# Performance work log

Measured on AMD Instinct MI355X. Metric: run time of the kernel, lower is better.

Reference implementation:

```python
import jax, jax.numpy as jnp
import numpy as np


def setup_inputs() -> dict:
    key = jax.random.key(0)
    k1, k2, k3, k4 = jax.random.split(key, 4)
    B, S, d_in, d_out = 4, 2048, 1024, 1024
    scale = 1.0 / np.sqrt(d_in)
    x = jax.random.normal(k1, (B, S, d_in), dtype=jnp.float32)
    # Linear weights stored as [d_in, d_out] so projection is x @ W
    Wq = jax.random.normal(k2, (d_in, d_out), dtype=jnp.float32) * scale
    Wk = jax.random.normal(k3, (d_in, d_out), dtype=jnp.float32) * scale
    Wv = jax.random.normal(k4, (d_in, d_out), dtype=jnp.float32) * scale
    return {"x": x, "Wq": Wq, "Wk": Wk, "Wv": Wv}


def reference(x, Wq, Wk, Wv):
    # QKV projections (no bias, matching qkv_bias=False)
    q = jnp.einsum("bsi,io->bso", x, Wq)
    k = jnp.einsum("bsi,io->bso", x, Wk)
    v = jnp.einsum("bsi,io->bso", x, Wv)
    d_k = k.shape[-1]
    # attn_scores = q @ k^T, causal mask (strict upper triangle -> -inf)
    scores = jnp.einsum("bqd,bkd->bqk", q, k)
    S = scores.shape[-1]
    causal = jnp.tril(jnp.ones((S, S), dtype=bool))  # True where allowed
    scores = jnp.where(causal, scores, -jnp.inf)
    attn = jax.nn.softmax(scores / jnp.sqrt(jnp.asarray(d_k, scores.dtype)), axis=-1)
    # dropout p=0.0 -> identity
    return jnp.einsum("bqk,bkd->bqd", attn, v)
```

## Files before the change

kernel.cpp:

```cpp
#include <hip/hip_runtime.h>

typedef _Float16 half8 __attribute__((ext_vector_type(8)));
typedef _Float16 half4 __attribute__((ext_vector_type(4)));
typedef float f32x4 __attribute__((ext_vector_type(4)));

#define ATT_SCALE 0.03125f
#define S_LEN 2048
#define D_DIM 1024
#define NB 4

__device__ __forceinline__ void async_cp16(const _Float16* g, _Float16* l)
{
    __builtin_amdgcn_global_load_lds(
        (const __attribute__((address_space(1))) void*)g,
        (__attribute__((address_space(3))) void*)l, 16, 0, 0);
}

__device__ __forceinline__ void gemm_core(const _Float16* __restrict__ Ag,
                                          const _Float16* __restrict__ Bg,
                                          int lda, int ldb, int ksteps,
                                          f32x4 acc[4][4])
{
    __shared__ _Float16 As[128 * 32];
    __shared__ _Float16 Bs[128 * 32];

    const int t    = threadIdx.x;
    const int wave = t >> 6;
    const int lane = t & 63;
    const int wm   = (wave >> 1) * 64;
    const int wn   = (wave & 1) * 64;
    const int lg   = lane >> 4;
    const int lr   = lane & 15;

    const int c0 = t,        r0 = c0 >> 2, h0 = (c0 & 3) * 8;
    const int c1 = 256 + t,  r1 = c1 >> 2, h1 = (c1 & 3) * 8;
    const int lb0 = (wave * 64) * 8;
    const int lb1 = (256 + wave * 64) * 8;

    const _Float16* a0p = Ag + (long)r0 * lda + h0;
    const _Float16* a1p = Ag + (long)r1 * lda + h1;
    const _Float16* b0p = Bg + (long)r0 * ldb + h0;
    const _Float16* b1p = Bg + (long)r1 * ldb + h1;

    for (int ks = 0; ks < ksteps; ++ks) {
        __syncthreads();
        async_cp16(a0p, As + lb0);
        async_cp16(a1p, As + lb1);
        async_cp16(b0p, Bs + lb0);
        async_cp16(b1p, Bs + lb1);
        __syncthreads();

        a0p += 32; a1p += 32; b0p += 32; b1p += 32;

        half8 af[4], bf[4];
#pragma unroll
        for (int i = 0; i < 4; ++i)
            af[i] = *(const half8*)&As[(wm + i * 16 + lr) * 32 + lg * 8];
#pragma unroll
        for (int j = 0; j < 4; ++j)
            bf[j] = *(const half8*)&Bs[(wn + j * 16 + lr) * 32 + lg * 8];

#pragma unroll
        for (int i = 0; i < 4; ++i)
#pragma unroll
            for (int j = 0; j < 4; ++j)
                acc[i][j] = __builtin_amdgcn_mfma_f32_16x16x32_f16(af[i], bf[j], acc[i][j], 0, 0, 0);
    }
}

__global__ void zero_sums_kernel(float* __restrict__ rs)
{
    rs[blockIdx.x * 256 + threadIdx.x] = 0.f;
}

__global__ void zero_out_kernel(float4* __restrict__ p, long n4)
{
    const float4 z = {0.f, 0.f, 0.f, 0.f};
    for (long i = (long)blockIdx.x * blockDim.x + threadIdx.x; i < n4;
         i += (long)gridDim.x * blockDim.x)
        p[i] = z;
}

__global__ void cast_x_kernel(const float* __restrict__ X, _Float16* __restrict__ Xh, int n)
{
    int i = blockIdx.x * blockDim.x + threadIdx.x;
    if (i * 4 >= n) return;
    float4 v = ((const float4*)X)[i];
    half4 h;
    h.x = (_Float16)v.x; h.y = (_Float16)v.y; h.z = (_Float16)v.z; h.w = (_Float16)v.w;
    ((half4*)Xh)[i] = h;
}

__global__ void transpose_w_kernel(const float* __restrict__ Wq,
                                   const float* __restrict__ Wk,
                                   const float* __restrict__ Wv,
                                   _Float16* __restrict__ Wt)
{
    __shared__ float tile[32][33];
    const int n0 = blockIdx.x * 32, k0 = blockIdx.y * 32, w = blockIdx.z;
    const float* Wsrc = (w == 0) ? Wq : (w == 1) ? Wk : Wv;
    _Float16* dst = Wt + (long)w * D_DIM * D_DIM;
    const int tx = threadIdx.x, ty = threadIdx.y;
#pragma unroll
    for (int j = 0; j < 4; ++j)
        tile[ty + 8 * j][tx] = Wsrc[(long)(k0 + ty + 8 * j) * D_DIM + n0 + tx];
    __syncthreads();
#pragma unroll
    for (int j = 0; j < 4; ++j)
        dst[(long)(n0 + ty + 8 * j) * D_DIM + k0 + tx] = (_Float16)tile[tx][ty + 8 * j];
}

__global__ __launch_bounds__(256) void proj_kernel(const _Float16* __restrict__ Xh,
                                                   const _Float16* __restrict__ Wt,
                                                   _Float16* __restrict__ Q,
                                                   _Float16* __restrict__ K,
                                                   _Float16* __restrict__ V)
{
    const int flat = blockIdx.x + 8 * (blockIdx.y + 64 * blockIdx.z);
    const int swz  = (flat & 7) * 192 + (flat >> 3);
    const int nt = swz & 7, mt = (swz >> 3) & 63, w = swz >> 9;

    f32x4 acc[4][4];
#pragma unroll
    for (int i = 0; i < 4; ++i)
#pragma unroll
        for (int j = 0; j < 4; ++j) acc[i][j] = (f32x4){0.f, 0.f, 0.f, 0.f};

    const _Float16* Ag = Xh + (long)mt * 128 * D_DIM;
    const _Float16* Bg = Wt + (long)w * D_DIM * D_DIM + (long)nt * 128 * D_DIM;
    gemm_core(Ag, Bg, D_DIM, D_DIM, D_DIM / 32, acc);

    _Float16* C = (w == 0) ? Q : (w == 1) ? K : V;
    const int t = threadIdx.x, wave = t >> 6, lane = t & 63;
    const int wm = (wave >> 1) * 64, wn = (wave & 1) * 64;
    const int lg = lane >> 4, lr = lane & 15;
    const long row0 = (long)mt * 128 + wm + 4 * lg;
    const long col0 = (long)nt * 128 + wn + lr;
#pragma unroll
    for (int i = 0; i < 4; ++i)
#pragma unroll
        for (int j = 0; j < 4; ++j)
#pragma unroll
            for (int r = 0; r < 4; ++r)
                C[(row0 + i * 16 + r) * D_DIM + col0 + j * 16] = (_Float16)acc[i][j][r];
}

__global__ __launch_bounds__(256) void transpose_v_kernel(const _Float16* __restrict__ V,
                                                          _Float16* __restrict__ Vt)
{
    __shared__ _Float16 tile[64][72];
    const int d0 = blockIdx.x * 64, s0 = blockIdx.y * 64;
    const long b = blockIdx.z;
    const _Float16* Vb = V + b * S_LEN * D_DIM;
    _Float16* Vtb = Vt + b * D_DIM * S_LEN;
    const int t = threadIdx.x;
    const int sr = t >> 3, c8 = (t & 7) * 8;

    *(half8*)&tile[sr][c8]      = *(const half8*)&Vb[(long)(s0 + sr) * D_DIM + d0 + c8];
    *(half8*)&tile[sr + 32][c8] = *(const half8*)&Vb[(long)(s0 + sr + 32) * D_DIM + d0 + c8];
    __syncthreads();

    const int dr = t >> 3, s8 = (t & 7) * 8;
    half8 o0, o1;
#pragma unroll
    for (int e = 0; e < 8; ++e) {
        o0[e] = tile[s8 + e][dr];
        o1[e] = tile[s8 + e][dr + 32];
    }
    *(half8*)&Vtb[(long)(d0 + dr) * S_LEN + s0 + s8]      = o0;
    *(half8*)&Vtb[(long)(d0 + dr + 32) * S_LEN + s0 + s8] = o1;
}

__global__ __launch_bounds__(256) void scores_exp_kernel(const _Float16* __restrict__ Q,
                                                         const _Float16* __restrict__ K,
                                                         _Float16* __restrict__ P,
                                                         float* __restrict__ row_sum)
{
    const int xcd = blockIdx.x & 7;
    const int idx = blockIdx.x >> 3;
    const int b   = idx / 17;
    const int l   = idx % 17;
    int qt, kt;
    if (l <= xcd) { qt = xcd;      kt = l; }
    else          { qt = 15 - xcd; kt = l - xcd - 1; }

    f32x4 acc[4][4];
#pragma unroll
    for (int i = 0; i < 4; ++i)
#pragma unroll
        for (int j = 0; j < 4; ++j) acc[i][j] = (f32x4){0.f, 0.f, 0.f, 0.f};

    const _Float16* Ag = Q + ((long)b * S_LEN + qt * 128) * D_DIM;
    const _Float16* Bg = K + ((long)b * S_LEN + kt * 128) * D_DIM;
    gemm_core(Ag, Bg, D_DIM, D_DIM, D_DIM / 32, acc);

    _Float16* Pb = P + (long)b * S_LEN * S_LEN;
    float* rsb = row_sum + (long)b * S_LEN;
    const int t = threadIdx.x, wave = t >> 6, lane = t & 63;
    const int wm = (wave >> 1) * 64, wn = (wave & 1) * 64;
    const int lg = lane >> 4, lr = lane & 15;
    const int row0 = qt * 128 + wm + 4 * lg;
    const int col0 = kt * 128 + wn + lr;

#pragma unroll
    for (int i = 0; i < 4; ++i) {
#pragma unroll
        for (int r = 0; r < 4; ++r) {
            const int row = row0 + i * 16 + r;
            float s = 0.f;
#pragma unroll
            for (int j = 0; j < 4; ++j) {
                const int col = col0 + j * 16;
                float p = (col <= row) ? __expf(acc[i][j][r] * ATT_SCALE) : 0.f;
                s += p;
                Pb[(long)row * S_LEN + col] = (_Float16)p;
            }
#pragma unroll
            for (int off = 1; off < 16; off <<= 1) s += __shfl_xor(s, off, 64);
            if (lr == 0) atomicAdd(&rsb[row], s);
        }
    }
}

__global__ __launch_bounds__(256) void pv_kernel(const _Float16* __restrict__ P,
                                                 const _Float16* __restrict__ Vt,
                                                 const float* __restrict__ row_sum,
                                                 float* __restrict__ O)
{
    const int xcd = blockIdx.x & 7;
    int r = blockIdx.x >> 3;
    const int b = r / 24;  r %= 24;
    const int j = r >> 3;
    const int nt = r & 7;
    const int sl = (j == 0) ? (7 - xcd) : (j == 1 ? 8 + 2 * xcd : 9 + 2 * xcd);

    int qt, k0s, ks;
    if (sl < 8) { qt = sl; k0s = 0; ks = (qt + 1) * 4; }
    else {
        const int e = sl - 8;
        qt = 8 + (e >> 1);
        ks = (qt + 1) * 2;
        k0s = (e & 1) * ks;
    }

    f32x4 acc[4][4];
#pragma unroll
    for (int i = 0; i < 4; ++i)
#pragma unroll
        for (int jj = 0; jj < 4; ++jj) acc[i][jj] = (f32x4){0.f, 0.f, 0.f, 0.f};

    const _Float16* Ag = P + ((long)b * S_LEN + qt * 128) * S_LEN + k0s * 32;
    const _Float16* Bg = Vt + (long)b * D_DIM * S_LEN + (long)nt * 128 * S_LEN + k0s * 32;
    gemm_core(Ag, Bg, S_LEN, S_LEN, ks, acc);

    float* Ob = O + (long)b * S_LEN * D_DIM;
    const float* rsb = row_sum + (long)b * S_LEN;
    const int t = threadIdx.x, wave = t >> 6, lane = t & 63;
    const int wm = (wave >> 1) * 64, wn = (wave & 1) * 64;
    const int lg = lane >> 4, lr = lane & 15;
    const long row0 = qt * 128 + wm + 4 * lg;
    const long col0 = (long)nt * 128 + wn + lr;

    if (sl < 8) {
#pragma unroll
        for (int i = 0; i < 4; ++i)
#pragma unroll
            for (int rr = 0; rr < 4; ++rr) {
                const float inv = 1.f / rsb[row0 + i * 16 + rr];
#pragma unroll
                for (int jj = 0; jj < 4; ++jj)
                    Ob[(row0 + i * 16 + rr) * D_DIM + col0 + jj * 16] = acc[i][jj][rr] * inv;
            }
    } else {
#pragma unroll
        for (int i = 0; i < 4; ++i)
#pragma unroll
            for (int rr = 0; rr < 4; ++rr) {
                const float inv = 1.f / rsb[row0 + i * 16 + rr];
#pragma unroll
                for (int jj = 0; jj < 4; ++jj)
                    atomicAdd(&Ob[(row0 + i * 16 + rr) * D_DIM + col0 + jj * 16],
                              acc[i][jj][rr] * inv);
            }
    }
}

extern "C" void kernel_launch(void* const* d_in, const int* in_sizes, int n_in,
                              void* d_out, int out_size, void* d_ws, size_t ws_size,
                              hipStream_t stream)
{
    const float* x  = (const float*)d_in[0];
    const float* Wq = (const float*)d_in[1];
    const float* Wk = (const float*)d_in[2];
    const float* Wv = (const float*)d_in[3];
    float* out = (float*)d_out;

    char* ws = (char*)d_ws;
    const long MiB = 1024 * 1024;
    _Float16* Q  = (_Float16*)(ws + 0 * MiB);
    _Float16* K  = (_Float16*)(ws + 16 * MiB);
    _Float16* V  = (_Float16*)(ws + 32 * MiB);
    _Float16* Vt = (_Float16*)(ws + 48 * MiB);
    _Float16* Xh = (_Float16*)(ws + 64 * MiB);
    _Float16* Wt = (_Float16*)(ws + 80 * MiB);
    _Float16* P  = (_Float16*)(ws + 86 * MiB);
    float*    RS = (float*)   (ws + 118 * MiB);

    const int nX = in_sizes[0];

    zero_sums_kernel<<<dim3(NB * S_LEN / 256), dim3(256), 0, stream>>>(RS);
    zero_out_kernel<<<dim3(2048), dim3(256), 0, stream>>>((float4*)out,
                                                          (long)NB * S_LEN * D_DIM / 4);
    cast_x_kernel<<<dim3((nX / 4 + 255) / 256), dim3(256), 0, stream>>>(x, Xh, nX);
    transpose_w_kernel<<<dim3(32, 32, 3), dim3(32, 8), 0, stream>>>(Wq, Wk, Wv, Wt);
    proj_kernel<<<dim3(8, 64, 3), dim3(256), 0, stream>>>(Xh, Wt, Q, K, V);
    transpose_v_kernel<<<dim3(16, 32, 4), dim3(256), 0, stream>>>(V, Vt);
    scores_exp_kernel<<<dim3(544), dim3(256), 0, stream>>>(Q, K, P, RS);
    pv_kernel<<<dim3(768), dim3(256), 0, stream>>>(P, Vt, RS, out);
}
```

Measured before the change: 187.6 us.

## Rewrite QKV projection GEMM with 256x256 tiles and double-buffered swizzled LDS

The projection kernel moves from a 128x128 tile with 256 threads to a 256x256 tile with 512 threads (8 waves). It stages 64-wide K slices through double-buffered LDS with async global-to-LDS copies and an XOR swizzle, raises wave priority around the MFMA bursts, and remaps blocks to improve L2 reuse. The goal is more arithmetic per byte loaded and load latency hidden behind MFMA work. In exchange it uses 128 KB of LDS and many more accumulator registers per block, and it launches only 384 blocks, which may leave some CUs without work.

```diff
diff --git a/kernel.cpp b/kernel.cpp
--- a/kernel.cpp
+++ b/kernel.cpp
@@ -110,39 +110,111 @@
         dst[(long)(n0 + ty + 8 * j) * D_DIM + k0 + tx] = (_Float16)tile[tx][ty + 8 * j];
 }
 
-__global__ __launch_bounds__(256) void proj_kernel(const _Float16* __restrict__ Xh,
-                                                   const _Float16* __restrict__ Wt,
-                                                   _Float16* __restrict__ Q,
-                                                   _Float16* __restrict__ K,
-                                                   _Float16* __restrict__ V)
-{
-    const int flat = blockIdx.x + 8 * (blockIdx.y + 64 * blockIdx.z);
-    const int swz  = (flat & 7) * 192 + (flat >> 3);
-    const int nt = swz & 7, mt = (swz >> 3) & 63, w = swz >> 9;
-
-    f32x4 acc[4][4];
-#pragma unroll
-    for (int i = 0; i < 4; ++i)
+__global__ __launch_bounds__(512, 2) void proj_kernel(const _Float16* __restrict__ Xh,
+                                                      const _Float16* __restrict__ Wt,
+                                                      _Float16* __restrict__ Q,
+                                                      _Float16* __restrict__ K,
+                                                      _Float16* __restrict__ V)
+{
+    __shared__ _Float16 As[2][256 * 64];
+    __shared__ _Float16 Bs[2][256 * 64];
+
+    const int bid = blockIdx.x;
+    const int g   = (bid & 7) * 48 + (bid >> 3);
+    const int mt  = g / 12;
+    const int rem = g % 12;
+    const int w   = rem >> 2;
+    const int nt  = rem & 3;
+
+    const int t    = threadIdx.x;
+    const int wave = t >> 6;
+    const int lane = t & 63;
+    const int wr   = wave >> 2;
+    const int wc   = wave & 3;
+    const int lg   = lane >> 4;
+    const int lr   = lane & 15;
+
+    const _Float16* Ag = Xh + (long)mt * 256 * D_DIM;
+    const _Float16* Bg = Wt + (long)w * D_DIM * D_DIM + (long)nt * 256 * D_DIM;
+
+    const int rsel = lane >> 3;
+    const int csel = ((lane & 7) ^ rsel) * 8;
+    const int w8   = wave * 8;
+    const int ldst = wave * 512;
+
+#define STAGE_TILE(dstA, dstB, kt1)                                             \
+    {                                                                           \
+        _Pragma("unroll")                                                       \
+        for (int i_ = 0; i_ < 4; ++i_)                                          \
+            async_cp16(Ag + (long)(i_ * 64 + w8 + rsel) * D_DIM + (kt1) * 64 + csel, \
+                       (dstA) + i_ * 4096 + ldst);                              \
+        _Pragma("unroll")                                                       \
+        for (int i_ = 0; i_ < 4; ++i_)                                          \
+            async_cp16(Bg + (long)(i_ * 64 + w8 + rsel) * D_DIM + (kt1) * 64 + csel, \
+                       (dstB) + i_ * 4096 + ldst);                              \
+    }
+
+    f32x4 acc[8][4];
+#pragma unroll
+    for (int i = 0; i < 8; ++i)
 #pragma unroll
         for (int j = 0; j < 4; ++j) acc[i][j] = (f32x4){0.f, 0.f, 0.f, 0.f};
 
-    const _Float16* Ag = Xh + (long)mt * 128 * D_DIM;
-    const _Float16* Bg = Wt + (long)w * D_DIM * D_DIM + (long)nt * 128 * D_DIM;
-    gemm_core(Ag, Bg, D_DIM, D_DIM, D_DIM / 32, acc);
+    STAGE_TILE(As[0], Bs[0], 0);
+
+    const int cswz = (lr & 7) << 4;
+    const int nkt  = D_DIM / 64;
+
+    for (int kt = 0; kt < nkt; ++kt) {
+        const int d = kt & 1;
+        if (kt > 0) __builtin_amdgcn_s_barrier();
+        if (kt + 1 < nkt) {
+            STAGE_TILE(As[d ^ 1], Bs[d ^ 1], kt + 1);
+            asm volatile("s_waitcnt vmcnt(8)" ::: "memory");
+        } else {
+            asm volatile("s_waitcnt vmcnt(0)" ::: "memory");
+        }
+        __builtin_amdgcn_s_barrier();
+
+        const char* Ab = (const char*)As[d];
+        const char* Bb = (const char*)Bs[d];
+#pragma unroll
+        for (int kh = 0; kh < 2; ++kh) {
+            const int cb = (kh * 64 + lg * 16) ^ cswz;
+            half8 bf[4];
+#pragma unroll
+            for (int j = 0; j < 4; ++j)
+                bf[j] = *(const half8*)(Bb + (wc * 64 + j * 16 + lr) * 128 + cb);
+#pragma unroll
+            for (int mh = 0; mh < 2; ++mh) {
+                half8 af[4];
+#pragma unroll
+                for (int i = 0; i < 4; ++i)
+                    af[i] = *(const half8*)(Ab + (wr * 128 + (mh * 4 + i) * 16 + lr) * 128 + cb);
+                __builtin_amdgcn_s_setprio(1);
+#pragma unroll
+                for (int i = 0; i < 4; ++i)
+#pragma unroll
+                    for (int j = 0; j < 4; ++j)
+                        acc[mh * 4 + i][j] = __builtin_amdgcn_mfma_f32_16x16x32_f16(
+                            af[i], bf[j], acc[mh * 4 + i][j], 0, 0, 0);
+                __builtin_amdgcn_s_setprio(0);
+                if (!(kh == 1 && mh == 1)) __builtin_amdgcn_s_barrier();
+            }
+        }
+    }
+#undef STAGE_TILE
 
     _Float16* C = (w == 0) ? Q : (w == 1) ? K : V;
-    const int t = threadIdx.x, wave = t >> 6, lane = t & 63;
-    const int wm = (wave >> 1) * 64, wn = (wave & 1) * 64;
-    const int lg = lane >> 4, lr = lane & 15;
-    const long row0 = (long)mt * 128 + wm + 4 * lg;
-    const long col0 = (long)nt * 128 + wn + lr;
-#pragma unroll
-    for (int i = 0; i < 4; ++i)
+    const long row0 = (long)mt * 256 + wr * 128 + lg * 4;
+    const long col0 = (long)nt * 256 + wc * 64 + lr;
+#pragma unroll
+    for (int mf = 0; mf < 8; ++mf)
 #pragma unroll
         for (int j = 0; j < 4; ++j)
 #pragma unroll
-            for (int r = 0; r < 4; ++r)
-                C[(row0 + i * 16 + r) * D_DIM + col0 + j * 16] = (_Float16)acc[i][j][r];
+            for (int rr = 0; rr < 4; ++rr)
+                C[(row0 + mf * 16 + rr) * D_DIM + col0 + j * 16] = (_Float16)acc[mf][j][rr];
 }
 
 __global__ __launch_bounds__(256) void transpose_v_kernel(const _Float16* __restrict__ V,
@@ -313,7 +385,7 @@
                                                           (long)NB * S_LEN * D_DIM / 4);
     cast_x_kernel<<<dim3((nX / 4 + 255) / 256), dim3(256), 0, stream>>>(x, Xh, nX);
     transpose_w_kernel<<<dim3(32, 32, 3), dim3(32, 8), 0, stream>>>(Wq, Wk, Wv, Wt);
-    proj_kernel<<<dim3(8, 64, 3), dim3(256), 0, stream>>>(Xh, Wt, Q, K, V);
+    proj_kernel<<<dim3(384), dim3(512), 0, stream>>>(Xh, Wt, Q, K, V);
     transpose_v_kernel<<<dim3(16, 32, 4), dim3(256), 0, stream>>>(V, Vt);
     scores_exp_kernel<<<dim3(544), dim3(256), 0, stream>>>(Q, K, P, RS);
     pv_kernel<<<dim3(768), dim3(256), 0, stream>>>(P, Vt, RS, out);
```

New measurement: 199.4 us. +6.3%, slower.

## Double GEMM K-tile to 64 with XOR-swizzled LDS and fuse init kernels

Applied to the files above, without the earlier changes.

The shared GEMM core now loads 64-wide K slices per iteration instead of 32. This halves the number of barrier pairs per tile and doubles the MFMA work between syncs. LDS rows are XOR-swizzled to avoid bank conflicts on the wider rows. The three init kernels (zero row sums, zero output, cast x) are merged into one launch, and the projection grid is flattened to 1D. The cost is twice the LDS use per block, which may lower occupancy.

```diff
diff --git a/kernel.cpp b/kernel.cpp
--- a/kernel.cpp
+++ b/kernel.cpp
@@ -16,13 +16,13 @@
         (__attribute__((address_space(3))) void*)l, 16, 0, 0);
 }
 
-__device__ __forceinline__ void gemm_core(const _Float16* __restrict__ Ag,
-                                          const _Float16* __restrict__ Bg,
-                                          int lda, int ldb, int ksteps,
-                                          f32x4 acc[4][4])
-{
-    __shared__ _Float16 As[128 * 32];
-    __shared__ _Float16 Bs[128 * 32];
+__device__ __forceinline__ void gemm_core64(const _Float16* __restrict__ Ag,
+                                            const _Float16* __restrict__ Bg,
+                                            int lda, int ldb, int ksteps64,
+                                            f32x4 acc[4][4])
+{
+    __shared__ _Float16 As[128 * 64];
+    __shared__ _Float16 Bs[128 * 64];
 
     const int t    = threadIdx.x;
     const int wave = t >> 6;
@@ -32,63 +32,72 @@
     const int lg   = lane >> 4;
     const int lr   = lane & 15;
 
-    const int c0 = t,        r0 = c0 >> 2, h0 = (c0 & 3) * 8;
-    const int c1 = 256 + t,  r1 = c1 >> 2, h1 = (c1 & 3) * 8;
-    const int lb0 = (wave * 64) * 8;
-    const int lb1 = (256 + wave * 64) * 8;
-
-    const _Float16* a0p = Ag + (long)r0 * lda + h0;
-    const _Float16* a1p = Ag + (long)r1 * lda + h1;
-    const _Float16* b0p = Bg + (long)r0 * ldb + h0;
-    const _Float16* b1p = Bg + (long)r1 * ldb + h1;
-
-    for (int ks = 0; ks < ksteps; ++ks) {
+    const int tr = t >> 3;
+    const int tc = ((t & 7) ^ (tr & 7)) * 8;
+    const int ldso = wave * 512;
+
+    const _Float16* ap0 = Ag + (long)(0 * 32 + tr) * lda + tc;
+    const _Float16* ap1 = Ag + (long)(1 * 32 + tr) * lda + tc;
+    const _Float16* ap2 = Ag + (long)(2 * 32 + tr) * lda + tc;
+    const _Float16* ap3 = Ag + (long)(3 * 32 + tr) * lda + tc;
+    const _Float16* bp0 = Bg + (long)(0 * 32 + tr) * ldb + tc;
+    const _Float16* bp1 = Bg + (long)(1 * 32 + tr) * ldb + tc;
+    const _Float16* bp2 = Bg + (long)(2 * 32 + tr) * ldb + tc;
+    const _Float16* bp3 = Bg + (long)(3 * 32 + tr) * ldb + tc;
+
+    const int arow = wm + lr;
+    const int brow = wn + lr;
+
+    for (int ks = 0; ks < ksteps64; ++ks) {
         __syncthreads();
-        async_cp16(a0p, As + lb0);
-        async_cp16(a1p, As + lb1);
-        async_cp16(b0p, Bs + lb0);
-        async_cp16(b1p, Bs + lb1);
+        async_cp16(ap0, As + 0 * 2048 + ldso);
+        async_cp16(ap1, As + 1 * 2048 + ldso);
+        async_cp16(ap2, As + 2 * 2048 + ldso);
+        async_cp16(ap3, As + 3 * 2048 + ldso);
+        async_cp16(bp0, Bs + 0 * 2048 + ldso);
+        async_cp16(bp1, Bs + 1 * 2048 + ldso);
+        async_cp16(bp2, Bs + 2 * 2048 + ldso);
+        async_cp16(bp3, Bs + 3 * 2048 + ldso);
         __syncthreads();
 
-        a0p += 32; a1p += 32; b0p += 32; b1p += 32;
-
-        half8 af[4], bf[4];
-#pragma unroll
-        for (int i = 0; i < 4; ++i)
-            af[i] = *(const half8*)&As[(wm + i * 16 + lr) * 32 + lg * 8];
-#pragma unroll
-        for (int j = 0; j < 4; ++j)
-            bf[j] = *(const half8*)&Bs[(wn + j * 16 + lr) * 32 + lg * 8];
-
-#pragma unroll
-        for (int i = 0; i < 4; ++i)
-#pragma unroll
-            for (int j = 0; j < 4; ++j)
-                acc[i][j] = __builtin_amdgcn_mfma_f32_16x16x32_f16(af[i], bf[j], acc[i][j], 0, 0, 0);
-    }
-}
-
-__global__ void zero_sums_kernel(float* __restrict__ rs)
-{
-    rs[blockIdx.x * 256 + threadIdx.x] = 0.f;
-}
-
-__global__ void zero_out_kernel(float4* __restrict__ p, long n4)
-{
-    const float4 z = {0.f, 0.f, 0.f, 0.f};
-    for (long i = (long)blockIdx.x * blockDim.x + threadIdx.x; i < n4;
-         i += (long)gridDim.x * blockDim.x)
-        p[i] = z;
-}
-
-__global__ void cast_x_kernel(const float* __restrict__ X, _Float16* __restrict__ Xh, int n)
-{
-    int i = blockIdx.x * blockDim.x + threadIdx.x;
-    if (i * 4 >= n) return;
+        ap0 += 64; ap1 += 64; ap2 += 64; ap3 += 64;
+        bp0 += 64; bp1 += 64; bp2 += 64; bp3 += 64;
+
+#pragma unroll
+        for (int kk = 0; kk < 2; ++kk) {
+            half8 af[4], bf[4];
+#pragma unroll
+            for (int mf = 0; mf < 4; ++mf) {
+                const int row = arow + mf * 16;
+                const int hof = (kk * 32 + lg * 8) ^ ((row & 7) * 8);
+                af[mf] = *(const half8*)&As[row * 64 + hof];
+            }
+#pragma unroll
+            for (int nf = 0; nf < 4; ++nf) {
+                const int row = brow + nf * 16;
+                const int hof = (kk * 32 + lg * 8) ^ ((row & 7) * 8);
+                bf[nf] = *(const half8*)&Bs[row * 64 + hof];
+            }
+#pragma unroll
+            for (int mf = 0; mf < 4; ++mf)
+#pragma unroll
+                for (int nf = 0; nf < 4; ++nf)
+                    acc[mf][nf] = __builtin_amdgcn_mfma_f32_16x16x32_f16(
+                        af[mf], bf[nf], acc[mf][nf], 0, 0, 0);
+        }
+    }
+}
+
+__global__ void init_kernel(const float* __restrict__ X, _Float16* __restrict__ Xh,
+                            float4* __restrict__ out, float* __restrict__ rs)
+{
+    const int i = blockIdx.x * 256 + threadIdx.x;
     float4 v = ((const float4*)X)[i];
     half4 h;
     h.x = (_Float16)v.x; h.y = (_Float16)v.y; h.z = (_Float16)v.z; h.w = (_Float16)v.w;
     ((half4*)Xh)[i] = h;
+    out[i] = (float4){0.f, 0.f, 0.f, 0.f};
+    if (i < NB * S_LEN) rs[i] = 0.f;
 }
 
 __global__ void transpose_w_kernel(const float* __restrict__ Wq,
@@ -116,7 +125,7 @@
                                                    _Float16* __restrict__ K,
                                                    _Float16* __restrict__ V)
 {
-    const int flat = blockIdx.x + 8 * (blockIdx.y + 64 * blockIdx.z);
+    const int flat = blockIdx.x;
     const int swz  = (flat & 7) * 192 + (flat >> 3);
     const int nt = swz & 7, mt = (swz >> 3) & 63, w = swz >> 9;
 
@@ -128,7 +137,7 @@
 
     const _Float16* Ag = Xh + (long)mt * 128 * D_DIM;
     const _Float16* Bg = Wt + (long)w * D_DIM * D_DIM + (long)nt * 128 * D_DIM;
-    gemm_core(Ag, Bg, D_DIM, D_DIM, D_DIM / 32, acc);
+    gemm_core64(Ag, Bg, D_DIM, D_DIM, D_DIM / 64, acc);
 
     _Float16* C = (w == 0) ? Q : (w == 1) ? K : V;
     const int t = threadIdx.x, wave = t >> 6, lane = t & 63;
@@ -192,7 +201,7 @@
 
     const _Float16* Ag = Q + ((long)b * S_LEN + qt * 128) * D_DIM;
     const _Float16* Bg = K + ((long)b * S_LEN + kt * 128) * D_DIM;
-    gemm_core(Ag, Bg, D_DIM, D_DIM, D_DIM / 32, acc);
+    gemm_core64(Ag, Bg, D_DIM, D_DIM, D_DIM / 64, acc);
 
     _Float16* Pb = P + (long)b * S_LEN * S_LEN;
     float* rsb = row_sum + (long)b * S_LEN;
@@ -234,13 +243,13 @@
     const int nt = r & 7;
     const int sl = (j == 0) ? (7 - xcd) : (j == 1 ? 8 + 2 * xcd : 9 + 2 * xcd);
 
-    int qt, k0s, ks;
-    if (sl < 8) { qt = sl; k0s = 0; ks = (qt + 1) * 4; }
+    int qt, k0, ks64;
+    if (sl < 8) { qt = sl; k0 = 0; ks64 = (qt + 1) * 2; }
     else {
         const int e = sl - 8;
         qt = 8 + (e >> 1);
-        ks = (qt + 1) * 2;
-        k0s = (e & 1) * ks;
+        ks64 = qt + 1;
+        k0 = (e & 1) * ks64 * 64;
     }
 
     f32x4 acc[4][4];
@@ -249,9 +258,9 @@
 #pragma unroll
         for (int jj = 0; jj < 4; ++jj) acc[i][jj] = (f32x4){0.f, 0.f, 0.f, 0.f};
 
-    const _Float16* Ag = P + ((long)b * S_LEN + qt * 128) * S_LEN + k0s * 32;
-    const _Float16* Bg = Vt + (long)b * D_DIM * S_LEN + (long)nt * 128 * S_LEN + k0s * 32;
-    gemm_core(Ag, Bg, S_LEN, S_LEN, ks, acc);
+    const _Float16* Ag = P + ((long)b * S_LEN + qt * 128) * S_LEN + k0;
+    const _Float16* Bg = Vt + (long)b * D_DIM * S_LEN + (long)nt * 128 * S_LEN + k0;
+    gemm_core64(Ag, Bg, S_LEN, S_LEN, ks64, acc);
 
     float* Ob = O + (long)b * S_LEN * D_DIM;
     const float* rsb = row_sum + (long)b * S_LEN;
@@ -306,14 +315,9 @@
     _Float16* P  = (_Float16*)(ws + 86 * MiB);
     float*    RS = (float*)   (ws + 118 * MiB);
 
-    const int nX = in_sizes[0];
-
-    zero_sums_kernel<<<dim3(NB * S_LEN / 256), dim3(256), 0, stream>>>(RS);
-    zero_out_kernel<<<dim3(2048), dim3(256), 0, stream>>>((float4*)out,
-                                                          (long)NB * S_LEN * D_DIM / 4);
-    cast_x_kernel<<<dim3((nX / 4 + 255) / 256), dim3(256), 0, stream>>>(x, Xh, nX);
+    init_kernel<<<dim3(8192), dim3(256), 0, stream>>>(x, Xh, (float4*)out, RS);
     transpose_w_kernel<<<dim3(32, 32, 3), dim3(32, 8), 0, stream>>>(Wq, Wk, Wv, Wt);
-    proj_kernel<<<dim3(8, 64, 3), dim3(256), 0, stream>>>(Xh, Wt, Q, K, V);
+    proj_kernel<<<dim3(1536), dim3(256), 0, stream>>>(Xh, Wt, Q, K, V);
     transpose_v_kernel<<<dim3(16, 32, 4), dim3(256), 0, stream>>>(V, Vt);
     scores_exp_kernel<<<dim3(544), dim3(256), 0, stream>>>(Q, K, P, RS);
     pv_kernel<<<dim3(768), dim3(256), 0, stream>>>(P, Vt, RS, out);
```

Measured after the change: 174.9 us. 6.7% less time.
